# Kernel optimization log

Hardware: AMD Instinct MI355X
Metric: run time of the kernel (lower is better)

The kernel has to match this reference:

```python
import jax, jax.numpy as jnp
import numpy as np

N_NODES = 50000
N_EDGES = 400000
IN_DIM = 128
HID_DIM = 128
OUT_DIM = 128


def setup_inputs() -> dict:
    key = jax.random.key(0)
    k_x, k_e, k_w1, k_b1, k_w2, k_b2 = jax.random.split(key, 6)
    x = jax.random.normal(k_x, (N_NODES, IN_DIM), dtype=jnp.float32)
    edge_index = jax.random.randint(k_e, (2, N_EDGES), 0, N_NODES, dtype=jnp.int64)
    # nn.Linear-style params: W is [out, in], kaiming-uniform-ish init
    lim1 = 1.0 / np.sqrt(IN_DIM)
    lim2 = 1.0 / np.sqrt(HID_DIM)
    W1 = jax.random.uniform(k_w1, (HID_DIM, IN_DIM), jnp.float32, -lim1, lim1)
    b1 = jax.random.uniform(k_b1, (HID_DIM,), jnp.float32, -lim1, lim1)
    W2 = jax.random.uniform(k_w2, (OUT_DIM, HID_DIM), jnp.float32, -lim2, lim2)
    b2 = jax.random.uniform(k_b2, (OUT_DIM,), jnp.float32, -lim2, lim2)
    return {"x": x, "edge_index": edge_index, "W1": W1, "b1": b1, "W2": W2, "b2": b2}


def reference(x, edge_index, W1, b1, W2, b2):
    # h = relu(fc1(x));  dropout in eval mode -> identity
    h = jax.nn.relu(x @ W1.T + b1)                      # [N, hid]
    src, dst = edge_index[0], edge_index[1]
    # gather messages from src, scatter-add (mean) into dst
    agg = jax.ops.segment_sum(h[src], dst, num_segments=N_NODES)      # [N, hid]
    deg = jax.ops.segment_sum(jnp.ones_like(dst, dtype=h.dtype), dst,
                              num_segments=N_NODES)                   # [N]
    deg = jnp.maximum(deg, 1.0)
    agg = agg / deg[:, None]
    # residual add + fc2
    return (agg + h) @ W2.T + b2                        # [N, out]
```

## Files before the change

### kernel.cpp

```cpp
#include <hip/hip_runtime.h>

#define N_NODES 50000
#define N_EDGES 400000
#define DIM 128
#define N_SCAN_BLK ((N_NODES + 255) / 256)
#define BUCKET_BLK ((N_EDGES + 255) / 256)
#define FC1_BLK ((N_NODES + 63) / 64)
#define AGG_BLK (N_NODES / 16)

typedef unsigned short u16;
typedef unsigned int   u32;
typedef __bf16 v8bf  __attribute__((ext_vector_type(8)));
typedef float  f32x4 __attribute__((ext_vector_type(4)));
typedef u16    u16x8 __attribute__((ext_vector_type(8)));

union BF8 { u16x8 u; v8bf b; };

__device__ __forceinline__ float bf2f(u16 u) {
    union { u32 i; float f; } v; v.i = ((u32)u) << 16; return v.f;
}
__device__ __forceinline__ u16 f2bf(float f) {
    union { float f; u32 i; } v; v.f = f; u32 u = v.i;
    return (u16)((u + 0x7FFFu + ((u >> 16) & 1u)) >> 16);
}

__global__ __launch_bounds__(256) void count_kernel(
    const int* __restrict__ edst, int* __restrict__ counts)
{
    int e = blockIdx.x * 256 + threadIdx.x;
    if (e >= N_EDGES) return;
    int dst = edst[e];
    if ((unsigned)dst >= N_NODES) return;
    atomicAdd(&counts[dst], 1);
}

__global__ __launch_bounds__(256) void scan_ticket_kernel(
    const int* __restrict__ counts, int* __restrict__ row_ptr,
    int* __restrict__ cursor, int* __restrict__ gcursor)
{
    __shared__ int tmp[256];
    __shared__ int sbase;
    const int t = threadIdx.x;
    const int i = blockIdx.x * 256 + t;
    int v = (i < N_NODES) ? counts[i] : 0;
    tmp[t] = v;
    __syncthreads();
#pragma unroll
    for (int ofs = 1; ofs < 256; ofs <<= 1) {
        int add = (t >= ofs) ? tmp[t - ofs] : 0;
        __syncthreads();
        tmp[t] += add;
        __syncthreads();
    }
    if (t == 255) sbase = atomicAdd(gcursor, tmp[255]);
    __syncthreads();
    if (i < N_NODES) {
        int r = sbase + tmp[t] - v;
        row_ptr[i] = r;
        cursor[i]  = r;
    }
}

__global__ __launch_bounds__(256, 3) void bucket_fc1_kernel(
    const int* __restrict__ esrc, const int* __restrict__ edst,
    int* __restrict__ cursor, int* __restrict__ esorted,
    const float* __restrict__ x, const float* __restrict__ W1,
    const float* __restrict__ b1, u16* __restrict__ h)
{
    __shared__ u16 xs[64 * 136];
    const int bid = blockIdx.x;

    if (bid < BUCKET_BLK) {
        int e = bid * 256 + threadIdx.x;
        if (e < N_EDGES) {
            int src = esrc[e], dst = edst[e];
            if ((unsigned)src < N_NODES && (unsigned)dst < N_NODES) {
                int pos = atomicAdd(&cursor[dst], 1);
                esorted[pos] = src;
            }
        }
        return;
    }

    const int t = threadIdx.x;
    const int wave = t >> 6, lane = t & 63, quad = lane >> 4, l15 = lane & 15;
    const int ch = wave >> 1, rh = wave & 1;
    const int row0 = (bid - BUCKET_BLK) * 64;

    BF8 barr[4][4];
#pragma unroll
    for (int ct = 0; ct < 4; ++ct)
#pragma unroll
        for (int ks = 0; ks < 4; ++ks) {
            const float* wp = W1 + (size_t)(ch * 64 + ct * 16 + l15) * DIM
                                 + ks * 32 + quad * 8;
            float4 f0 = *(const float4*)wp;
            float4 f1 = *(const float4*)(wp + 4);
            u16x8 p;
            p[0] = f2bf(f0.x); p[1] = f2bf(f0.y); p[2] = f2bf(f0.z); p[3] = f2bf(f0.w);
            p[4] = f2bf(f1.x); p[5] = f2bf(f1.y); p[6] = f2bf(f1.z); p[7] = f2bf(f1.w);
            barr[ct][ks].u = p;
        }

    {
        int srow = t >> 2, k0 = (t & 3) * 32;
        int grow = row0 + srow; if (grow >= N_NODES) grow = N_NODES - 1;
        const float* xp = x + (size_t)grow * DIM + k0;
#pragma unroll
        for (int j = 0; j < 4; ++j) {
            float4 f0 = *(const float4*)(xp + j * 8);
            float4 f1 = *(const float4*)(xp + j * 8 + 4);
            u16x8 p;
            p[0] = f2bf(f0.x); p[1] = f2bf(f0.y); p[2] = f2bf(f0.z); p[3] = f2bf(f0.w);
            p[4] = f2bf(f1.x); p[5] = f2bf(f1.y); p[6] = f2bf(f1.z); p[7] = f2bf(f1.w);
            *(u16x8*)&xs[srow * 136 + k0 + j * 8] = p;
        }
    }

    f32x4 acc[2][4];
#pragma unroll
    for (int ct = 0; ct < 4; ++ct) {
        float bv = b1[ch * 64 + ct * 16 + l15];
        acc[0][ct] = (f32x4){bv, bv, bv, bv};
        acc[1][ct] = (f32x4){bv, bv, bv, bv};
    }
    __syncthreads();

#pragma unroll
    for (int ks = 0; ks < 4; ++ks) {
        BF8 a0, a1;
        a0.u = *(const u16x8*)&xs[(rh * 32 +  0 + l15) * 136 + ks * 32 + quad * 8];
        a1.u = *(const u16x8*)&xs[(rh * 32 + 16 + l15) * 136 + ks * 32 + quad * 8];
#pragma unroll
        for (int ct = 0; ct < 4; ++ct) {
            acc[0][ct] = __builtin_amdgcn_mfma_f32_16x16x32_bf16(
                a0.b, barr[ct][ks].b, acc[0][ct], 0, 0, 0);
            acc[1][ct] = __builtin_amdgcn_mfma_f32_16x16x32_bf16(
                a1.b, barr[ct][ks].b, acc[1][ct], 0, 0, 0);
        }
    }

#pragma unroll
    for (int rt = 0; rt < 2; ++rt)
#pragma unroll
        for (int i = 0; i < 4; ++i) {
            int row = row0 + rh * 32 + rt * 16 + quad * 4 + i;
            if (row < N_NODES) {
#pragma unroll
                for (int ct = 0; ct < 4; ++ct) {
                    int col = ch * 64 + ct * 16 + l15;
                    h[(size_t)row * DIM + col] = f2bf(fmaxf(acc[rt][ct][i], 0.f));
                }
            }
        }
}

__global__ __launch_bounds__(256) void agg_fc2_kernel(
    const int* __restrict__ row_ptr, const int* __restrict__ counts,
    const int* __restrict__ esorted, const u16* __restrict__ h,
    const float* __restrict__ W2, const float* __restrict__ b2,
    float* __restrict__ out)
{
    __shared__ u16 xs[16 * 136];
    const int t = threadIdx.x;
    const int wv = t >> 6, lane = t & 63, quad = lane >> 4, l15 = lane & 15;
    const int row0 = blockIdx.x * 16;

    {
        const int s = wv * 4 + quad;
        const int n = row0 + s;
        const int start = row_ptr[n];
        const int deg   = counts[n];
        const int end   = start + deg;

        float a[8];
#pragma unroll
        for (int j = 0; j < 8; ++j) a[j] = 0.f;

        int e = start;
        for (; e + 8 <= end; e += 8) {
            int s0 = esorted[e + 0], s1 = esorted[e + 1];
            int s2 = esorted[e + 2], s3 = esorted[e + 3];
            int s4 = esorted[e + 4], s5 = esorted[e + 5];
            int s6 = esorted[e + 6], s7 = esorted[e + 7];
            u16x8 v0 = *(const u16x8*)(h + (size_t)s0 * DIM + l15 * 8);
            u16x8 v1 = *(const u16x8*)(h + (size_t)s1 * DIM + l15 * 8);
            u16x8 v2 = *(const u16x8*)(h + (size_t)s2 * DIM + l15 * 8);
            u16x8 v3 = *(const u16x8*)(h + (size_t)s3 * DIM + l15 * 8);
            u16x8 v4 = *(const u16x8*)(h + (size_t)s4 * DIM + l15 * 8);
            u16x8 v5 = *(const u16x8*)(h + (size_t)s5 * DIM + l15 * 8);
            u16x8 v6 = *(const u16x8*)(h + (size_t)s6 * DIM + l15 * 8);
            u16x8 v7 = *(const u16x8*)(h + (size_t)s7 * DIM + l15 * 8);
#pragma unroll
            for (int j = 0; j < 8; ++j) {
                a[j] += bf2f(v0[j]); a[j] += bf2f(v1[j]);
                a[j] += bf2f(v2[j]); a[j] += bf2f(v3[j]);
                a[j] += bf2f(v4[j]); a[j] += bf2f(v5[j]);
                a[j] += bf2f(v6[j]); a[j] += bf2f(v7[j]);
            }
        }
        for (; e + 4 <= end; e += 4) {
            int s0 = esorted[e + 0], s1 = esorted[e + 1];
            int s2 = esorted[e + 2], s3 = esorted[e + 3];
            u16x8 v0 = *(const u16x8*)(h + (size_t)s0 * DIM + l15 * 8);
            u16x8 v1 = *(const u16x8*)(h + (size_t)s1 * DIM + l15 * 8);
            u16x8 v2 = *(const u16x8*)(h + (size_t)s2 * DIM + l15 * 8);
            u16x8 v3 = *(const u16x8*)(h + (size_t)s3 * DIM + l15 * 8);
#pragma unroll
            for (int j = 0; j < 8; ++j) {
                a[j] += bf2f(v0[j]); a[j] += bf2f(v1[j]);
                a[j] += bf2f(v2[j]); a[j] += bf2f(v3[j]);
            }
        }
        for (; e < end; ++e) {
            u16x8 v = *(const u16x8*)(h + (size_t)esorted[e] * DIM + l15 * 8);
#pragma unroll
            for (int j = 0; j < 8; ++j) a[j] += bf2f(v[j]);
        }

        u16x8 hres = *(const u16x8*)(h + (size_t)n * DIM + l15 * 8);
        float inv = (deg > 0) ? 1.f / (float)deg : 1.f;
        u16x8 pk;
#pragma unroll
        for (int j = 0; j < 8; ++j)
            pk[j] = f2bf(a[j] * inv + bf2f(hres[j]));
        *(u16x8*)&xs[s * 136 + l15 * 8] = pk;
    }

    BF8 barr[2][4];
#pragma unroll
    for (int ct = 0; ct < 2; ++ct)
#pragma unroll
        for (int ks = 0; ks < 4; ++ks) {
            const float* wp = W2 + (size_t)(wv * 32 + ct * 16 + l15) * DIM
                                 + ks * 32 + quad * 8;
            float4 f0 = *(const float4*)wp;
            float4 f1 = *(const float4*)(wp + 4);
            u16x8 p;
            p[0] = f2bf(f0.x); p[1] = f2bf(f0.y); p[2] = f2bf(f0.z); p[3] = f2bf(f0.w);
            p[4] = f2bf(f1.x); p[5] = f2bf(f1.y); p[6] = f2bf(f1.z); p[7] = f2bf(f1.w);
            barr[ct][ks].u = p;
        }

    f32x4 acc[2];
#pragma unroll
    for (int ct = 0; ct < 2; ++ct) {
        float bv = b2[wv * 32 + ct * 16 + l15];
        acc[ct] = (f32x4){bv, bv, bv, bv};
    }
    __syncthreads();

#pragma unroll
    for (int ks = 0; ks < 4; ++ks) {
        BF8 a0;
        a0.u = *(const u16x8*)&xs[l15 * 136 + ks * 32 + quad * 8];
#pragma unroll
        for (int ct = 0; ct < 2; ++ct) {
            acc[ct] = __builtin_amdgcn_mfma_f32_16x16x32_bf16(
                a0.b, barr[ct][ks].b, acc[ct], 0, 0, 0);
        }
    }

#pragma unroll
    for (int i = 0; i < 4; ++i) {
        int row = row0 + quad * 4 + i;
#pragma unroll
        for (int ct = 0; ct < 2; ++ct) {
            int col = wv * 32 + ct * 16 + l15;
            out[(size_t)row * DIM + col] = acc[ct][i];
        }
    }
}

extern "C" void kernel_launch(void* const* d_in, const int* in_sizes, int n_in,
                              void* d_out, int out_size, void* d_ws, size_t ws_size,
                              hipStream_t stream)
{
    const float* x  = (const float*)d_in[0];
    const int*   ei = (const int*)d_in[1];
    const float* W1 = (const float*)d_in[2];
    const float* b1 = (const float*)d_in[3];
    const float* W2 = (const float*)d_in[4];
    const float* b2 = (const float*)d_in[5];
    float* out = (float*)d_out;

    const int* esrc = ei;
    const int* edst = ei + N_EDGES;

    char* ws = (char*)d_ws;
    size_t off = 0;
    u16* h       = (u16*)(ws + off); off += (size_t)N_NODES * DIM * 2;
    int* counts  = (int*)(ws + off); off += (size_t)N_NODES * 4;
    int* gcursor = (int*)(ws + off); off += 4;
    int* row_ptr = (int*)(ws + off); off += (size_t)N_NODES * 4;
    int* cursor  = (int*)(ws + off); off += (size_t)N_NODES * 4;
    int* esorted = (int*)(ws + off); off += (size_t)N_EDGES * 4;

    hipMemsetAsync(counts, 0, (size_t)(N_NODES + 1) * 4, stream);

    count_kernel<<<BUCKET_BLK, 256, 0, stream>>>(edst, counts);
    scan_ticket_kernel<<<N_SCAN_BLK, 256, 0, stream>>>(
        counts, row_ptr, cursor, gcursor);
    bucket_fc1_kernel<<<BUCKET_BLK + FC1_BLK, 256, 0, stream>>>(
        esrc, edst, cursor, esorted, x, W1, b1, h);
    agg_fc2_kernel<<<AGG_BLK, 256, 0, stream>>>(
        row_ptr, counts, esorted, h, W2, b2, out);
}
```

Before: 187.2 us.

## Record per-edge slot during counting and scatter without atomics after scan

Counting now returns each edge's occurrence index from the atomicAdd and stores it in an occ array; this count runs fused with fc1 in one launch. A new atomic-free scatter kernel then places edges at row_ptr[dst]+occ[e], and the cursor array is removed. This drops the second pass of atomics on cursor. The cost is an extra 400K-entry int array written and read back, and fc1 no longer overlaps the scatter. The residual h load in the aggregation kernel is also moved before the gather loop.

```diff
diff --git a/kernel.cpp b/kernel.cpp
--- a/kernel.cpp
+++ b/kernel.cpp
@@ -24,46 +24,9 @@
     return (u16)((u + 0x7FFFu + ((u >> 16) & 1u)) >> 16);
 }
 
-__global__ __launch_bounds__(256) void count_kernel(
-    const int* __restrict__ edst, int* __restrict__ counts)
-{
-    int e = blockIdx.x * 256 + threadIdx.x;
-    if (e >= N_EDGES) return;
-    int dst = edst[e];
-    if ((unsigned)dst >= N_NODES) return;
-    atomicAdd(&counts[dst], 1);
-}
-
-__global__ __launch_bounds__(256) void scan_ticket_kernel(
-    const int* __restrict__ counts, int* __restrict__ row_ptr,
-    int* __restrict__ cursor, int* __restrict__ gcursor)
-{
-    __shared__ int tmp[256];
-    __shared__ int sbase;
-    const int t = threadIdx.x;
-    const int i = blockIdx.x * 256 + t;
-    int v = (i < N_NODES) ? counts[i] : 0;
-    tmp[t] = v;
-    __syncthreads();
-#pragma unroll
-    for (int ofs = 1; ofs < 256; ofs <<= 1) {
-        int add = (t >= ofs) ? tmp[t - ofs] : 0;
-        __syncthreads();
-        tmp[t] += add;
-        __syncthreads();
-    }
-    if (t == 255) sbase = atomicAdd(gcursor, tmp[255]);
-    __syncthreads();
-    if (i < N_NODES) {
-        int r = sbase + tmp[t] - v;
-        row_ptr[i] = r;
-        cursor[i]  = r;
-    }
-}
-
-__global__ __launch_bounds__(256, 3) void bucket_fc1_kernel(
+__global__ __launch_bounds__(256, 3) void count_fc1_kernel(
     const int* __restrict__ esrc, const int* __restrict__ edst,
-    int* __restrict__ cursor, int* __restrict__ esorted,
+    int* __restrict__ counts, int* __restrict__ occ,
     const float* __restrict__ x, const float* __restrict__ W1,
     const float* __restrict__ b1, u16* __restrict__ h)
 {
@@ -74,10 +37,8 @@
         int e = bid * 256 + threadIdx.x;
         if (e < N_EDGES) {
             int src = esrc[e], dst = edst[e];
-            if ((unsigned)src < N_NODES && (unsigned)dst < N_NODES) {
-                int pos = atomicAdd(&cursor[dst], 1);
-                esorted[pos] = src;
-            }
+            if ((unsigned)src < N_NODES && (unsigned)dst < N_NODES)
+                occ[e] = atomicAdd(&counts[dst], 1);
         }
         return;
     }
@@ -155,6 +116,41 @@
         }
 }
 
+__global__ __launch_bounds__(256) void scan_ticket_kernel(
+    const int* __restrict__ counts, int* __restrict__ row_ptr,
+    int* __restrict__ gcursor)
+{
+    __shared__ int tmp[256];
+    __shared__ int sbase;
+    const int t = threadIdx.x;
+    const int i = blockIdx.x * 256 + t;
+    int v = (i < N_NODES) ? counts[i] : 0;
+    tmp[t] = v;
+    __syncthreads();
+#pragma unroll
+    for (int ofs = 1; ofs < 256; ofs <<= 1) {
+        int add = (t >= ofs) ? tmp[t - ofs] : 0;
+        __syncthreads();
+        tmp[t] += add;
+        __syncthreads();
+    }
+    if (t == 255) sbase = atomicAdd(gcursor, tmp[255]);
+    __syncthreads();
+    if (i < N_NODES) row_ptr[i] = sbase + tmp[t] - v;
+}
+
+__global__ __launch_bounds__(256) void scatter_kernel(
+    const int* __restrict__ esrc, const int* __restrict__ edst,
+    const int* __restrict__ occ, const int* __restrict__ row_ptr,
+    int* __restrict__ esorted)
+{
+    int e = blockIdx.x * 256 + threadIdx.x;
+    if (e >= N_EDGES) return;
+    int src = esrc[e], dst = edst[e];
+    if ((unsigned)src < N_NODES && (unsigned)dst < N_NODES)
+        esorted[row_ptr[dst] + occ[e]] = src;
+}
+
 __global__ __launch_bounds__(256) void agg_fc2_kernel(
     const int* __restrict__ row_ptr, const int* __restrict__ counts,
     const int* __restrict__ esorted, const u16* __restrict__ h,
@@ -172,6 +168,8 @@
         const int start = row_ptr[n];
         const int deg   = counts[n];
         const int end   = start + deg;
+
+        u16x8 hres = *(const u16x8*)(h + (size_t)n * DIM + l15 * 8);
 
         float a[8];
 #pragma unroll
@@ -218,7 +216,6 @@
             for (int j = 0; j < 8; ++j) a[j] += bf2f(v[j]);
         }
 
-        u16x8 hres = *(const u16x8*)(h + (size_t)n * DIM + l15 * 8);
         float inv = (deg > 0) ? 1.f / (float)deg : 1.f;
         u16x8 pk;
 #pragma unroll
@@ -293,16 +290,17 @@
     int* counts  = (int*)(ws + off); off += (size_t)N_NODES * 4;
     int* gcursor = (int*)(ws + off); off += 4;
     int* row_ptr = (int*)(ws + off); off += (size_t)N_NODES * 4;
-    int* cursor  = (int*)(ws + off); off += (size_t)N_NODES * 4;
+    int* occ     = (int*)(ws + off); off += (size_t)N_EDGES * 4;
     int* esorted = (int*)(ws + off); off += (size_t)N_EDGES * 4;
 
     hipMemsetAsync(counts, 0, (size_t)(N_NODES + 1) * 4, stream);
 
-    count_kernel<<<BUCKET_BLK, 256, 0, stream>>>(edst, counts);
+    count_fc1_kernel<<<BUCKET_BLK + FC1_BLK, 256, 0, stream>>>(
+        esrc, edst, counts, occ, x, W1, b1, h);
     scan_ticket_kernel<<<N_SCAN_BLK, 256, 0, stream>>>(
-        counts, row_ptr, cursor, gcursor);
-    bucket_fc1_kernel<<<BUCKET_BLK + FC1_BLK, 256, 0, stream>>>(
-        esrc, edst, cursor, esorted, x, W1, b1, h);
+        counts, row_ptr, gcursor);
+    scatter_kernel<<<BUCKET_BLK, 256, 0, stream>>>(
+        esrc, edst, occ, row_ptr, esorted);
     agg_fc2_kernel<<<AGG_BLK, 256, 0, stream>>>(
         row_ptr, counts, esorted, h, W2, b2, out);
 }
```

Result: faster. 175.7 us (-6.2%).
